# Performance work log

Hardware: AMD Instinct MI355X
Metric: run time of the kernel (lower is better)

Reference implementation:

```python
import jax, jax.numpy as jnp
import numpy as np

DN = ('NCHW', 'OIHW', 'NCHW')
HEADS = 4
EPS_LN = 1e-5
EPS_NORM = 1e-12


def conv(x, w, pad=0, groups=1):
    return jax.lax.conv_general_dilated(
        x, w, window_strides=(1, 1), padding=[(pad, pad), (pad, pad)],
        dimension_numbers=DN, feature_group_count=groups)


def layernorm(x, w, b):
    # LayerNorm over channel axis per spatial position (to_3d -> LN(c) -> to_4d)
    mu = jnp.mean(x, axis=1, keepdims=True)
    var = jnp.mean((x - mu) ** 2, axis=1, keepdims=True)
    return (x - mu) / jnp.sqrt(var + EPS_LN) * w[None, :, None, None] + b[None, :, None, None]


def setup_inputs() -> dict:
    key = jax.random.key(0)
    ks = jax.random.split(key, 12)
    b, dim, h, w = 2, 192, 128, 128
    hidden = int(dim * 2.66)  # 510

    def rn(k, shape, scale=0.05):
        return jax.random.normal(k, shape, dtype=jnp.float32) * scale

    return {
        'x': jax.random.normal(ks[0], (b, dim, h, w), dtype=jnp.float32),
        'illum': jax.random.normal(ks[1], (b, dim, h, w), dtype=jnp.float32),
        'ln1_w': jnp.ones((dim,), jnp.float32), 'ln1_b': jnp.zeros((dim,), jnp.float32),
        'lnL_w': jnp.ones((dim,), jnp.float32), 'lnL_b': jnp.zeros((dim,), jnp.float32),
        'ln2_w': jnp.ones((dim,), jnp.float32), 'ln2_b': jnp.zeros((dim,), jnp.float32),
        'q_w': rn(ks[2], (dim, dim, 1, 1)),
        'qdw_w': rn(ks[3], (dim, dim, 3, 3)),        # full 3x3 conv (no groups in source)
        'kv_w': rn(ks[4], (2 * dim, dim, 1, 1)),
        'kvdw_w': rn(ks[5], (2 * dim, 1, 3, 3)),     # depthwise, groups = 2*dim
        'temp': jnp.ones((HEADS, 1, 1), jnp.float32),
        'proj_w': rn(ks[6], (dim, dim, 1, 1)),
        'pin_w': rn(ks[7], (hidden, dim, 1, 1)),
        'dw_w': rn(ks[8], (hidden, hidden, 3, 3)),   # full 3x3 conv (no groups in source)
        'pout_w': rn(ks[9], (dim, hidden, 1, 1)),
    }


def _block(x, illum, ln1_w, ln1_b, lnL_w, lnL_b, ln2_w, ln2_b,
           q_w, qdw_w, kv_w, kvdw_w, temp, proj_w, pin_w, dw_w, pout_w):
    b, c, h, w = x.shape
    ch = c // HEADS

    # ---- Illum-guided channel attention (MDTA) ----
    xn = layernorm(x, ln1_w, ln1_b)
    iln = layernorm(illum, lnL_w, lnL_b)
    q = conv(conv(iln, q_w), qdw_w, pad=1)
    kv = conv(conv(xn, kv_w), kvdw_w, pad=1, groups=2 * c)
    k, v = jnp.split(kv, 2, axis=1)

    def split_heads(t):
        return t.reshape(b, HEADS, ch, h * w)  # b head c (hw)

    q, k, v = split_heads(q), split_heads(k), split_heads(v)
    q = q / jnp.maximum(jnp.linalg.norm(q, axis=-1, keepdims=True), EPS_NORM)
    k = k / jnp.maximum(jnp.linalg.norm(k, axis=-1, keepdims=True), EPS_NORM)

    attn = jnp.einsum('bhce,bhde->bhcd', q, k) * temp[None]  # [b, head, ch, ch]
    attn = jax.nn.softmax(attn, axis=-1)
    out = jnp.einsum('bhcd,bhde->bhce', attn, v).reshape(b, c, h, w)
    x = x + conv(out, proj_w)

    # ---- FFN: 1x1 -> full 3x3 -> GELU -> 1x1 ----
    xn2 = layernorm(x, ln2_w, ln2_b)
    f = conv(xn2, pin_w)
    f = jax.nn.gelu(conv(f, dw_w, pad=1), approximate=False)
    x = x + conv(f, pout_w)
    return x


def reference(x, illum, ln1_w, ln1_b, lnL_w, lnL_b, ln2_w, ln2_b,
              q_w, qdw_w, kv_w, kvdw_w, temp, proj_w, pin_w, dw_w, pout_w):
    return _block(x, illum, ln1_w, ln1_b, lnL_w, lnL_b, ln2_w, ln2_b,
                  q_w, qdw_w, kv_w, kvdw_w, temp, proj_w, pin_w, dw_w, pout_w)
```

## Files before the change

kernel.cpp:

```cpp
#include <hip/hip_runtime.h>
#include <hip/hip_bf16.h>

typedef __hip_bfloat16 bf16;
typedef __attribute__((ext_vector_type(8))) short bf16x8v;
typedef __attribute__((ext_vector_type(4))) float f32x4;

namespace {
constexpr int B_  = 2;
constexpr int C_  = 192;
constexpr int HW_ = 128 * 128;
constexpr int C2_ = 384;
}

static __device__ __forceinline__ float fb(bf16 v) { return __bfloat162float(v); }
static __device__ __forceinline__ bf16 tob(float v) { return __float2bfloat16(v); }

typedef __attribute__((address_space(1))) const char GChar;
typedef __attribute__((address_space(3))) char LChar;
static __device__ __forceinline__ void gl16(const void* g, void* l) {
    __builtin_amdgcn_global_load_lds((GChar*)g, (LChar*)l, 16, 0, 0);
}
static __device__ __forceinline__ bf16x8v lread(const bf16* base, int row, int slot) {
    const char* p = (const char*)base + (size_t)row * 128 + ((size_t)((slot ^ (row & 7))) << 4);
    return *(const bf16x8v*)p;
}

static __device__ __forceinline__ void rp1(const float* W, bf16* Wr, int blk, int t,
                                           int N, int K, int Npad, int Kpad) {
    int i = blk * 256 + t;
    if (i >= Npad * Kpad) return;
    int n = i / Kpad, k = i % Kpad;
    float v = (n < N && k < K) ? W[n * K + k] : 0.f;
    Wr[i] = tob(v);
}
static __device__ __forceinline__ void rp3(const float* W, bf16* Wr, int blk, int t,
                                           int N, int K, int Npad, int Kpad) {
    int i = blk * 256 + t;
    int NK = Npad * Kpad;
    if (i >= NK) return;
    int n = i / Kpad, k = i % Kpad;
    if (n < N && k < K) {
        const float* src = W + ((size_t)(n * K + k)) * 9;
#pragma unroll
        for (int q = 0; q < 9; q++) Wr[(size_t)q * NK + i] = tob(src[q]);
    } else {
#pragma unroll
        for (int q = 0; q < 9; q++) Wr[(size_t)q * NK + i] = tob(0.f);
    }
}
__global__ __launch_bounds__(256) void k_repack_all(
    const float* __restrict__ qw, const float* __restrict__ kvw,
    const float* __restrict__ projw, const float* __restrict__ pinw,
    const float* __restrict__ poutw, const float* __restrict__ qdww,
    const float* __restrict__ dww,
    bf16* __restrict__ Wq1, bf16* __restrict__ Wkv, bf16* __restrict__ Wproj,
    bf16* __restrict__ Wpin, bf16* __restrict__ Wpout, bf16* __restrict__ Wqdw,
    bf16* __restrict__ Wdw, char* __restrict__ zpage) {
    int blk = blockIdx.x, t = threadIdx.x;
    if (blk < 144)        rp1(qw,    Wq1,   blk,        t, 192, 192, 192, 192);
    else if (blk < 432)   rp1(kvw,   Wkv,   blk - 144,  t, 384, 192, 384, 192);
    else if (blk < 576)   rp1(projw, Wproj, blk - 432,  t, 192, 192, 192, 192);
    else if (blk < 960)   rp1(pinw,  Wpin,  blk - 576,  t, 510, 192, 512, 192);
    else if (blk < 1344)  rp1(poutw, Wpout, blk - 960,  t, 192, 510, 192, 512);
    else if (blk < 1488)  rp3(qdww,  Wqdw,  blk - 1344, t, 192, 192, 192, 192);
    else if (blk < 2512)  rp3(dww,   Wdw,   blk - 1488, t, 510, 510, 512, 512);
    else ((uint4*)zpage)[t] = make_uint4(0u, 0u, 0u, 0u);
}

__global__ __launch_bounds__(256) void k_ln_nchw(const float* __restrict__ X0,
                                                 const float* __restrict__ X1,
                                                 const float* __restrict__ w0,
                                                 const float* __restrict__ b0,
                                                 const float* __restrict__ w1,
                                                 const float* __restrict__ b1,
                                                 bf16* __restrict__ out0,
                                                 bf16* __restrict__ out1) {
    const float* X = blockIdx.y ? X1 : X0;
    const float* w = blockIdx.y ? w1 : w0;
    const float* bb = blockIdx.y ? b1 : b0;
    bf16* out = blockIdx.y ? out1 : out0;
    __shared__ float lds[64][C_ + 1];
    int t = threadIdx.x;
    int p0 = blockIdx.x * 64;
    int b = p0 / HW_, pi0 = p0 % HW_;
    for (int i = t; i < 64 * C_; i += 256) {
        int c = i >> 6, pp = i & 63;
        lds[pp][c] = X[((size_t)(b * C_ + c)) * HW_ + pi0 + pp];
    }
    __syncthreads();
    int pp = t >> 2, qq = t & 3;
    float s = 0.f, s2 = 0.f;
    for (int c = qq * 48; c < qq * 48 + 48; c++) { float v = lds[pp][c]; s += v; s2 += v * v; }
    s  += __shfl_xor(s, 1);  s  += __shfl_xor(s, 2);
    s2 += __shfl_xor(s2, 1); s2 += __shfl_xor(s2, 2);
    float mu = s / C_;
    float rstd = rsqrtf(s2 / C_ - mu * mu + 1e-5f);
    size_t ob = ((size_t)(p0 + pp)) * C_;
    for (int c = qq * 48; c < qq * 48 + 48; c++)
        out[ob + c] = tob((lds[pp][c] - mu) * rstd * w[c] + bb[c]);
}

__global__ __launch_bounds__(256) void k_ln_pc(const bf16* __restrict__ X2,
                                               const float* __restrict__ w,
                                               const float* __restrict__ bb,
                                               bf16* __restrict__ out) {
    int t = threadIdx.x;
    int p = blockIdx.x * 64 + (t >> 2), qq = t & 3;
    const bf16* row = X2 + (size_t)p * C_;
    float s = 0.f, s2 = 0.f;
    for (int c = qq * 48; c < qq * 48 + 48; c++) { float v = fb(row[c]); s += v; s2 += v * v; }
    s  += __shfl_xor(s, 1);  s  += __shfl_xor(s, 2);
    s2 += __shfl_xor(s2, 1); s2 += __shfl_xor(s2, 2);
    float mu = s / C_;
    float rstd = rsqrtf(s2 / C_ - mu * mu + 1e-5f);
    bf16* orow = out + (size_t)p * C_;
    for (int c = qq * 48; c < qq * 48 + 48; c++)
        orow[c] = tob((fb(row[c]) - mu) * rstd * w[c] + bb[c]);
}

template <int BN, int EPI>
__global__ __launch_bounds__(256) void k_gemm1x1(const bf16* __restrict__ A,
                                                 const bf16* __restrict__ Wr,
                                                 const int K, const int Cout,
                                                 void* __restrict__ outp,
                                                 const void* __restrict__ resid,
                                                 const int wbstride) {
    constexpr int WN = BN / 2, FN = WN / 16, BIT = BN / 32;
    __shared__ __align__(16) bf16 As[128 * 64];
    __shared__ __align__(16) bf16 Bs[BN * 64];
    const int t = threadIdx.x;
    const int mt = blockIdx.x;
    const int n0 = blockIdx.y * BN;
    const int b = mt >> 7, y = mt & 127;
    const int w = t >> 6, lane = t & 63;
    const int wm = w >> 1, wn = w & 1;
    const int g = lane >> 4, r = lane & 15;
    const int ldw = t - lane;

    f32x4 acc[4][FN];
#pragma unroll
    for (int i = 0; i < 4; i++)
#pragma unroll
        for (int j = 0; j < FN; j++) acc[i][j] = {0.f, 0.f, 0.f, 0.f};

    const bf16* Abase = A + (size_t)mt * 128 * K;
    const bf16* Wbase = Wr + (size_t)b * wbstride;

    for (int c0 = 0; c0 < K; c0 += 64) {
#pragma unroll
        for (int it = 0; it < 4; it++) {
            int idx = it * 256 + t;
            int row = idx >> 3, sl = idx & 7;
            const char* gp = (const char*)(Abase + (size_t)row * K + c0) + ((sl ^ (row & 7)) << 4);
            gl16(gp, (char*)As + (size_t)(it * 256 + ldw) * 16);
        }
#pragma unroll
        for (int it = 0; it < BIT; it++) {
            int idx = it * 256 + t;
            int row = idx >> 3, sl = idx & 7;
            const char* gp = (const char*)(Wbase + (size_t)(n0 + row) * K + c0) + ((sl ^ (row & 7)) << 4);
            gl16(gp, (char*)Bs + (size_t)(it * 256 + ldw) * 16);
        }
        __syncthreads();
#pragma unroll
        for (int ks = 0; ks < 2; ks++) {
            bf16x8v af[4], bv[FN];
#pragma unroll
            for (int fm = 0; fm < 4; fm++)
                af[fm] = lread(As, wm * 64 + fm * 16 + r, ks * 4 + g);
#pragma unroll
            for (int fn = 0; fn < FN; fn++)
                bv[fn] = lread(Bs, wn * WN + fn * 16 + r, ks * 4 + g);
#pragma unroll
            for (int fm = 0; fm < 4; fm++)
#pragma unroll
                for (int fn = 0; fn < FN; fn++)
                    acc[fm][fn] = __builtin_amdgcn_mfma_f32_16x16x32_bf16(af[fm], bv[fn], acc[fm][fn], 0, 0, 0);
        }
        __syncthreads();
    }

#pragma unroll
    for (int fm = 0; fm < 4; fm++)
#pragma unroll
        for (int fn = 0; fn < FN; fn++)
#pragma unroll
            for (int reg = 0; reg < 4; reg++) {
                int xl = wm * 64 + fm * 16 + g * 4 + reg;
                int co = n0 + wn * WN + fn * 16 + r;
                float v = acc[fm][fn][reg];
                if constexpr (EPI == 1) {
                    ((bf16*)outp)[((size_t)mt * 128 + xl) * Cout + co] = tob(v);
                } else if constexpr (EPI == 2) {
                    v += ((const float*)resid)[((size_t)(b * C_ + co)) * HW_ + y * 128 + xl];
                    ((bf16*)outp)[((size_t)mt * 128 + xl) * C_ + co] = tob(v);
                } else {
                    v += fb(((const bf16*)resid)[((size_t)mt * 128 + xl) * C_ + co]);
                    ((float*)outp)[((size_t)(b * C_ + co)) * HW_ + y * 128 + xl] = v;
                }
            }
}

template <int BN, int EPI>
__global__ __launch_bounds__(256) void k_gemm3x3(const bf16* __restrict__ A,
                                                 const bf16* __restrict__ Wr,
                                                 const int Cin, const int Cout,
                                                 bf16* __restrict__ outp,
                                                 const char* __restrict__ zpage) {
    constexpr int WN = BN / 2, FN = WN / 16, BIT = BN / 32;
    __shared__ __align__(16) bf16 As[160 * 64];
    __shared__ __align__(16) bf16 Bs[BN * 64];
    const int t = threadIdx.x;
    const int mtRaw = blockIdx.x;
    const int mt = ((mtRaw & 7) << 5) | (mtRaw >> 3);
    const int n0 = blockIdx.y * BN;
    const int b = mt >> 7, y = mt & 127;
    const int w = t >> 6, lane = t & 63;
    const int wm = w >> 1, wn = w & 1;
    const int g = lane >> 4, r = lane & 15;
    const int ldw = t - lane;

    f32x4 acc[4][FN];
#pragma unroll
    for (int i = 0; i < 4; i++)
#pragma unroll
        for (int j = 0; j < FN; j++) acc[i][j] = {0.f, 0.f, 0.f, 0.f};

    for (int ky = 0; ky < 3; ky++) {
        const int yy = y + ky - 1;
        if (yy < 0 || yy > 127) continue;
        const bf16* Ab = A + ((size_t)b * HW_ + (size_t)yy * 128) * Cin;
        for (int c0 = 0; c0 < Cin; c0 += 64) {
            for (int kx = 0; kx < 3; kx++) {
                if (kx == 0) {
#pragma unroll
                    for (int it = 0; it < 5; it++) {
                        int idx = it * 256 + t;
                        int row = idx >> 3, sl = idx & 7;
                        int so = (sl ^ (row & 7)) << 4;
                        const char* gp = (row >= 1 && row <= 128)
                            ? (const char*)(Ab + (size_t)(row - 1) * Cin + c0) + so
                            : zpage + so;
                        gl16(gp, (char*)As + (size_t)(it * 256 + ldw) * 16);
                    }
                }
                const bf16* Wb = Wr + (size_t)(ky * 3 + kx) * Cout * Cin;
#pragma unroll
                for (int it = 0; it < BIT; it++) {
                    int idx = it * 256 + t;
                    int row = idx >> 3, sl = idx & 7;
                    const char* gp = (const char*)(Wb + (size_t)(n0 + row) * Cin + c0) + ((sl ^ (row & 7)) << 4);
                    gl16(gp, (char*)Bs + (size_t)(it * 256 + ldw) * 16);
                }
                __syncthreads();
#pragma unroll
                for (int ks = 0; ks < 2; ks++) {
                    bf16x8v af[4], bv[FN];
#pragma unroll
                    for (int fm = 0; fm < 4; fm++)
                        af[fm] = lread(As, wm * 64 + fm * 16 + r + kx, ks * 4 + g);
#pragma unroll
                    for (int fn = 0; fn < FN; fn++)
                        bv[fn] = lread(Bs, wn * WN + fn * 16 + r, ks * 4 + g);
#pragma unroll
                    for (int fm = 0; fm < 4; fm++)
#pragma unroll
                        for (int fn = 0; fn < FN; fn++)
                            acc[fm][fn] = __builtin_amdgcn_mfma_f32_16x16x32_bf16(af[fm], bv[fn], acc[fm][fn], 0, 0, 0);
                }
                __syncthreads();
            }
        }
    }
#pragma unroll
    for (int fm = 0; fm < 4; fm++)
#pragma unroll
        for (int fn = 0; fn < FN; fn++)
#pragma unroll
            for (int reg = 0; reg < 4; reg++) {
                int xl = wm * 64 + fm * 16 + g * 4 + reg;
                int co = n0 + wn * WN + fn * 16 + r;
                float v = acc[fm][fn][reg];
                if constexpr (EPI == 1) v = 0.5f * v * (1.0f + erff(v * 0.70710678118654752f));
                outp[((size_t)mt * 128 + xl) * Cout + co] = tob(v);
            }
}

__global__ __launch_bounds__(192) void k_dwconv2(const bf16* __restrict__ kv,
                                                 const float* __restrict__ wdw,
                                                 bf16* __restrict__ kout,
                                                 bf16* __restrict__ vout) {
    __shared__ float wlds[1728];
    const int t = threadIdx.x;
    const int row = blockIdx.x;
    const int z = blockIdx.y;
    const int b = row >> 7, y = row & 127;
    for (int i = t; i < 432; i += 192)
        ((float4*)wlds)[i] = ((const float4*)(wdw + (size_t)z * 1728))[i];
    __syncthreads();
    const int c8h = t % 24, xg = t / 24;
    const int cbase = z * C_ + c8h * 8;
    float wreg[9][8];
#pragma unroll
    for (int tap = 0; tap < 9; tap++)
#pragma unroll
        for (int j = 0; j < 8; j++) wreg[tap][j] = wlds[(c8h * 8 + j) * 9 + tap];

    bf16* outb = (z == 0 ? kout : vout) + (size_t)(b * HW_ + y * 128) * C_ + c8h * 8;
    const uint4 zero4 = make_uint4(0u, 0u, 0u, 0u);
    for (int i = 0; i < 16; i++) {
        int x = xg + 8 * i;
        float acc[8];
#pragma unroll
        for (int j = 0; j < 8; j++) acc[j] = 0.f;
#pragma unroll
        for (int ky = 0; ky < 3; ky++) {
            int yy = y + ky - 1;
            if (yy < 0 || yy > 127) continue;
            const bf16* rb = kv + ((size_t)b * HW_ + (size_t)yy * 128) * C2_ + cbase;
#pragma unroll
            for (int kx = 0; kx < 3; kx++) {
                int xx = x + kx - 1;
                uint4 vv = (xx >= 0 && xx <= 127) ? *(const uint4*)(rb + (size_t)xx * C2_) : zero4;
                const bf16* pv = (const bf16*)&vv;
#pragma unroll
                for (int j = 0; j < 8; j++)
                    acc[j] += fb(pv[j]) * wreg[ky * 3 + kx][j];
            }
        }
        union { bf16 h[8]; uint4 u; } ov;
#pragma unroll
        for (int j = 0; j < 8; j++) ov.h[j] = tob(acc[j]);
        *(uint4*)(outb + (size_t)x * C_) = ov.u;
    }
}

__global__ __launch_bounds__(192) void k_ssqpart(const bf16* __restrict__ q,
                                                 const bf16* __restrict__ k,
                                                 float* __restrict__ ssq) {
    __shared__ float red[192][8];
    int t = threadIdx.x;
    int c8 = t % 24, slot = t / 24;
    int ch = blockIdx.x, b = blockIdx.y, sel = blockIdx.z;
    const bf16* src = (sel ? k : q) + ((size_t)b * HW_ + ch * 256) * C_ + c8 * 8;
    float s[8];
#pragma unroll
    for (int j = 0; j < 8; j++) s[j] = 0.f;
    for (int i = slot; i < 256; i += 8) {
        uint4 v = *(const uint4*)(src + (size_t)i * C_);
        const bf16* pv = (const bf16*)&v;
#pragma unroll
        for (int j = 0; j < 8; j++) { float x = fb(pv[j]); s[j] += x * x; }
    }
#pragma unroll
    for (int j = 0; j < 8; j++) red[t][j] = s[j];
    __syncthreads();
    if (slot == 0) {
        float o[8];
#pragma unroll
        for (int j = 0; j < 8; j++) o[j] = 0.f;
        for (int ss = 0; ss < 8; ss++)
#pragma unroll
            for (int j = 0; j < 8; j++) o[j] += red[c8 + 24 * ss][j];
        float* dst = ssq + (((size_t)(sel * 2 + b)) * 64 + ch) * C_ + c8 * 8;
#pragma unroll
        for (int j = 0; j < 8; j++) dst[j] = o[j];
    }
}

__global__ __launch_bounds__(256) void k_qk(const bf16* __restrict__ q,
                                            const bf16* __restrict__ k,
                                            float* __restrict__ Spart) {
    __shared__ float qs[64][49];
    __shared__ float ks[64][49];
    int t = threadIdx.x;
    int ch = blockIdx.x, hd = blockIdx.y, b = blockIdx.z;
    int i0 = (t >> 4) * 3, j0 = (t & 15) * 3;
    float acc[3][3];
#pragma unroll
    for (int a = 0; a < 3; a++)
#pragma unroll
        for (int c = 0; c < 3; c++) acc[a][c] = 0.f;

    for (int sub = 0; sub < 4; sub++) {
        size_t rbase = ((size_t)b * HW_ + ch * 256 + sub * 64) * C_ + hd * 48;
        for (int i = t; i < 64 * 6; i += 256) {
            int row = i / 6, oc = i % 6;
            uint4 v = *(const uint4*)(q + rbase + (size_t)row * C_ + oc * 8);
            const bf16* pv = (const bf16*)&v;
#pragma unroll
            for (int j = 0; j < 8; j++) qs[row][oc * 8 + j] = fb(pv[j]);
            uint4 v2 = *(const uint4*)(k + rbase + (size_t)row * C_ + oc * 8);
            const bf16* pv2 = (const bf16*)&v2;
#pragma unroll
            for (int j = 0; j < 8; j++) ks[row][oc * 8 + j] = fb(pv2[j]);
        }
        __syncthreads();
        for (int p = 0; p < 64; p++) {
            float a0 = qs[p][i0], a1 = qs[p][i0 + 1], a2 = qs[p][i0 + 2];
            float b0 = ks[p][j0], b1 = ks[p][j0 + 1], b2 = ks[p][j0 + 2];
            acc[0][0] += a0 * b0; acc[0][1] += a0 * b1; acc[0][2] += a0 * b2;
            acc[1][0] += a1 * b0; acc[1][1] += a1 * b1; acc[1][2] += a1 * b2;
            acc[2][0] += a2 * b0; acc[2][1] += a2 * b1; acc[2][2] += a2 * b2;
        }
        __syncthreads();
    }
    float* dst = Spart + (((size_t)(b * 4 + hd)) * 64 + ch) * 2304;
#pragma unroll
    for (int a = 0; a < 3; a++)
#pragma unroll
        for (int c = 0; c < 3; c++) dst[(i0 + a) * 48 + (j0 + c)] = acc[a][c];
}

__global__ __launch_bounds__(256) void k_softmax(const float* __restrict__ Spart,
                                                 const float* __restrict__ ssq,
                                                 const float* __restrict__ temp,
                                                 bf16* __restrict__ attnW) {
    __shared__ float S[2304];
    __shared__ float invk_s[48];
    int t = threadIdx.x;
    int hd = blockIdx.x, b = blockIdx.y;
    const float* base = Spart + ((size_t)(b * 4 + hd)) * 64 * 2304;
    for (int e = t; e < 2304; e += 256) {
        float s = 0.f;
        for (int ch = 0; ch < 64; ch++) s += base[(size_t)ch * 2304 + e];
        S[e] = s;
    }
    if (t < 48) {
        int c = hd * 48 + t;
        float sk = 0.f;
        for (int ch = 0; ch < 64; ch++) sk += ssq[((size_t)(2 + b) * 64 + ch) * C_ + c];
        invk_s[t] = 1.f / fmaxf(sqrtf(sk), 1e-12f);
    }
    __syncthreads();
    if (t >= 48) return;
    int c = hd * 48 + t;
    float sq = 0.f;
    for (int ch = 0; ch < 64; ch++) sq += ssq[((size_t)b * 64 + ch) * C_ + c];
    float qi = 1.f / fmaxf(sqrtf(sq), 1e-12f);
    float tp = temp[hd];
    float row[48];
    float mx = -1e30f;
    for (int j = 0; j < 48; j++) {
        float s = S[t * 48 + j] * qi * invk_s[j] * tp;
        row[j] = s;
        mx = fmaxf(mx, s);
    }
    float sum = 0.f;
    for (int j = 0; j < 48; j++) { row[j] = expf(row[j] - mx); sum += row[j]; }
    float is = 1.f / sum;
    bf16* wrow = attnW + ((size_t)b * 192 + hd * 48 + t) * 192;
    for (int blk4 = 0; blk4 < 4; blk4++)
        for (int j = 0; j < 48; j++)
            wrow[blk4 * 48 + j] = tob(blk4 == hd ? row[j] * is : 0.f);
}

extern "C" void kernel_launch(void* const* d_in, const int* in_sizes, int n_in,
                              void* d_out, int out_size, void* d_ws, size_t ws_size,
                              hipStream_t stream) {
    const float* x     = (const float*)d_in[0];
    const float* illum = (const float*)d_in[1];
    const float* ln1w  = (const float*)d_in[2];
    const float* ln1b  = (const float*)d_in[3];
    const float* lnLw  = (const float*)d_in[4];
    const float* lnLb  = (const float*)d_in[5];
    const float* ln2w  = (const float*)d_in[6];
    const float* ln2b  = (const float*)d_in[7];
    const float* qw    = (const float*)d_in[8];
    const float* qdww  = (const float*)d_in[9];
    const float* kvw   = (const float*)d_in[10];
    const float* kvdww = (const float*)d_in[11];
    const float* temp  = (const float*)d_in[12];
    const float* projw = (const float*)d_in[13];
    const float* pinw  = (const float*)d_in[14];
    const float* dww   = (const float*)d_in[15];
    const float* poutw = (const float*)d_in[16];

    char* ws = (char*)d_ws;
    bf16*  Wq1   = (bf16*)(ws + 0);
    bf16*  Wkv   = (bf16*)(ws + 73728);
    bf16*  Wqdw  = (bf16*)(ws + 221184);
    bf16*  Wproj = (bf16*)(ws + 884736);
    bf16*  Wpin  = (bf16*)(ws + 958464);
    bf16*  Wdw   = (bf16*)(ws + 1155072);
    bf16*  Wpout = (bf16*)(ws + 5873664);
    float* ssq   = (float*)(ws + 6070272);
    char*  zpage = (char*)(ws + 6266880);
    const size_t A0 = 6270976, u = 12582912;
    bf16* xn    = (bf16*)(ws + A0 + 0 * u);
    bf16* iln   = (bf16*)(ws + A0 + 1 * u);
    bf16* qtmp  = (bf16*)(ws + A0 + 2 * u);
    bf16* qb    = (bf16*)(ws + A0 + 1 * u);
    bf16* kvtmp = (bf16*)(ws + A0 + 2 * u);
    bf16* kb    = (bf16*)(ws + A0 + 0 * u);
    bf16* vb    = (bf16*)(ws + A0 + 4 * u);
    float* Spart = (float*)(ws + A0 + 3 * u);
    bf16*  attnW = (bf16*)(ws + A0 + 3 * u + 4718592);
    bf16* outa  = (bf16*)(ws + A0 + 2 * u);
    bf16* x2    = (bf16*)(ws + A0 + 0 * u);
    bf16* xn2   = (bf16*)(ws + A0 + 3 * u);
    bf16* fbuf  = (bf16*)(ws + A0 + 4 * u);
    bf16* gbuf  = (bf16*)(ws + A0 + 1 * u);

    k_repack_all<<<2513, 256, 0, stream>>>(qw, kvw, projw, pinw, poutw, qdww, dww,
                                           Wq1, Wkv, Wproj, Wpin, Wpout, Wqdw, Wdw, zpage);

    k_ln_nchw<<<dim3(512, 2), 256, 0, stream>>>(x, illum, ln1w, ln1b, lnLw, lnLb, xn, iln);

    k_gemm1x1<96, 1><<<dim3(256, 2), 256, 0, stream>>>(iln, Wq1, 192, 192, qtmp, nullptr, 0);
    k_gemm3x3<96, 0><<<dim3(256, 2), 256, 0, stream>>>(qtmp, Wqdw, 192, 192, qb, zpage);

    k_gemm1x1<128, 1><<<dim3(256, 3), 256, 0, stream>>>(xn, Wkv, 192, 384, kvtmp, nullptr, 0);
    k_dwconv2<<<dim3(256, 2), 192, 0, stream>>>(kvtmp, kvdww, kb, vb);

    k_ssqpart<<<dim3(64, 2, 2), 192, 0, stream>>>(qb, kb, ssq);
    k_qk<<<dim3(64, 4, 2), 256, 0, stream>>>(qb, kb, Spart);
    k_softmax<<<dim3(4, 2), 256, 0, stream>>>(Spart, ssq, temp, attnW);
    k_gemm1x1<96, 1><<<dim3(256, 2), 256, 0, stream>>>(vb, attnW, 192, 192, outa, nullptr, 36864);

    k_gemm1x1<96, 2><<<dim3(256, 2), 256, 0, stream>>>(outa, Wproj, 192, 192, x2, x, 0);

    k_ln_pc<<<512, 256, 0, stream>>>(x2, ln2w, ln2b, xn2);
    k_gemm1x1<128, 1><<<dim3(256, 4), 256, 0, stream>>>(xn2, Wpin, 192, 512, fbuf, nullptr, 0);
    k_gemm3x3<128, 1><<<dim3(256, 4), 256, 0, stream>>>(fbuf, Wdw, 512, 512, gbuf, zpage);
    k_gemm1x1<96, 3><<<dim3(256, 2), 256, 0, stream>>>(gbuf, Wpout, 512, 192, d_out, x2, 0);
}
```

Baseline: 406.6 us.

## Vectorize layernorm I/O, slide dwconv window, fuse sum-of-squares into qk kernel

Layernorm kernels now read the NCHW input as float4, keep the bf16 per-channel rows in registers, and write 16-byte packed bf16 stores instead of scalar accesses. The depthwise conv gives each thread a contiguous run of 16 pixels and keeps a 3x3 register window that slides along x, so each input vector is loaded once instead of three times. The separate q/k sum-of-squares kernel is removed and its reduction is folded into k_qk, which already stages the same tiles in LDS. This saves one launch and a full re-read of q and k, at the cost of a little extra LDS work and another barrier inside k_qk.

```diff
diff --git a/kernel.cpp b/kernel.cpp
--- a/kernel.cpp
+++ b/kernel.cpp
@@ -83,9 +83,11 @@
     int t = threadIdx.x;
     int p0 = blockIdx.x * 64;
     int b = p0 / HW_, pi0 = p0 % HW_;
-    for (int i = t; i < 64 * C_; i += 256) {
-        int c = i >> 6, pp = i & 63;
-        lds[pp][c] = X[((size_t)(b * C_ + c)) * HW_ + pi0 + pp];
+    for (int i = t; i < 64 * C_ / 4; i += 256) {
+        int c = i >> 4, pp4 = (i & 15) << 2;
+        float4 v = *(const float4*)(X + ((size_t)(b * C_ + c)) * HW_ + pi0 + pp4);
+        lds[pp4 + 0][c] = v.x; lds[pp4 + 1][c] = v.y;
+        lds[pp4 + 2][c] = v.z; lds[pp4 + 3][c] = v.w;
     }
     __syncthreads();
     int pp = t >> 2, qq = t & 3;
@@ -95,9 +97,17 @@
     s2 += __shfl_xor(s2, 1); s2 += __shfl_xor(s2, 2);
     float mu = s / C_;
     float rstd = rsqrtf(s2 / C_ - mu * mu + 1e-5f);
-    size_t ob = ((size_t)(p0 + pp)) * C_;
-    for (int c = qq * 48; c < qq * 48 + 48; c++)
-        out[ob + c] = tob((lds[pp][c] - mu) * rstd * w[c] + bb[c]);
+    bf16* ob = out + ((size_t)(p0 + pp)) * C_ + qq * 48;
+#pragma unroll
+    for (int j = 0; j < 6; j++) {
+        union { bf16 h[8]; uint4 u; } ov;
+#pragma unroll
+        for (int e = 0; e < 8; e++) {
+            int c = qq * 48 + j * 8 + e;
+            ov.h[e] = tob((lds[pp][c] - mu) * rstd * w[c] + bb[c]);
+        }
+        *(uint4*)(ob + j * 8) = ov.u;
+    }
 }
 
 __global__ __launch_bounds__(256) void k_ln_pc(const bf16* __restrict__ X2,
@@ -106,16 +116,33 @@
                                                bf16* __restrict__ out) {
     int t = threadIdx.x;
     int p = blockIdx.x * 64 + (t >> 2), qq = t & 3;
-    const bf16* row = X2 + (size_t)p * C_;
+    const bf16* row = X2 + (size_t)p * C_ + qq * 48;
+    uint4 u[6];
+#pragma unroll
+    for (int j = 0; j < 6; j++) u[j] = *(const uint4*)(row + j * 8);
     float s = 0.f, s2 = 0.f;
-    for (int c = qq * 48; c < qq * 48 + 48; c++) { float v = fb(row[c]); s += v; s2 += v * v; }
+#pragma unroll
+    for (int j = 0; j < 6; j++) {
+        const bf16* pv = (const bf16*)&u[j];
+#pragma unroll
+        for (int e = 0; e < 8; e++) { float v = fb(pv[e]); s += v; s2 += v * v; }
+    }
     s  += __shfl_xor(s, 1);  s  += __shfl_xor(s, 2);
     s2 += __shfl_xor(s2, 1); s2 += __shfl_xor(s2, 2);
     float mu = s / C_;
     float rstd = rsqrtf(s2 / C_ - mu * mu + 1e-5f);
-    bf16* orow = out + (size_t)p * C_;
-    for (int c = qq * 48; c < qq * 48 + 48; c++)
-        orow[c] = tob((fb(row[c]) - mu) * rstd * w[c] + bb[c]);
+    bf16* orow = out + (size_t)p * C_ + qq * 48;
+#pragma unroll
+    for (int j = 0; j < 6; j++) {
+        const bf16* pv = (const bf16*)&u[j];
+        union { bf16 h[8]; uint4 u4; } ov;
+#pragma unroll
+        for (int e = 0; e < 8; e++) {
+            int c = qq * 48 + j * 8 + e;
+            ov.h[e] = tob((fb(pv[e]) - mu) * rstd * w[c] + bb[c]);
+        }
+        *(uint4*)(orow + j * 8) = ov.u4;
+    }
 }
 
 template <int BN, int EPI>
@@ -308,75 +335,60 @@
 
     bf16* outb = (z == 0 ? kout : vout) + (size_t)(b * HW_ + y * 128) * C_ + c8h * 8;
     const uint4 zero4 = make_uint4(0u, 0u, 0u, 0u);
+    const int x0 = xg * 16;
+    bool vy[3]; const bf16* rowp[3];
+#pragma unroll
+    for (int ky = 0; ky < 3; ky++) {
+        int yy = y + ky - 1;
+        vy[ky] = (yy >= 0 && yy <= 127);
+        int yyc = vy[ky] ? yy : 0;
+        rowp[ky] = kv + ((size_t)b * HW_ + (size_t)yyc * 128) * C2_ + cbase;
+    }
+    uint4 win[3][3];
+#pragma unroll
+    for (int ky = 0; ky < 3; ky++) {
+        win[ky][0] = (vy[ky] && x0 - 1 >= 0) ? *(const uint4*)(rowp[ky] + (size_t)(x0 - 1) * C2_) : zero4;
+        win[ky][1] = vy[ky] ? *(const uint4*)(rowp[ky] + (size_t)x0 * C2_) : zero4;
+    }
     for (int i = 0; i < 16; i++) {
-        int x = xg + 8 * i;
+        int x = x0 + i;
+#pragma unroll
+        for (int ky = 0; ky < 3; ky++)
+            win[ky][2] = (vy[ky] && x + 1 <= 127) ? *(const uint4*)(rowp[ky] + (size_t)(x + 1) * C2_) : zero4;
         float acc[8];
 #pragma unroll
         for (int j = 0; j < 8; j++) acc[j] = 0.f;
 #pragma unroll
-        for (int ky = 0; ky < 3; ky++) {
-            int yy = y + ky - 1;
-            if (yy < 0 || yy > 127) continue;
-            const bf16* rb = kv + ((size_t)b * HW_ + (size_t)yy * 128) * C2_ + cbase;
+        for (int ky = 0; ky < 3; ky++)
 #pragma unroll
             for (int kx = 0; kx < 3; kx++) {
-                int xx = x + kx - 1;
-                uint4 vv = (xx >= 0 && xx <= 127) ? *(const uint4*)(rb + (size_t)xx * C2_) : zero4;
-                const bf16* pv = (const bf16*)&vv;
+                const bf16* pv = (const bf16*)&win[ky][kx];
 #pragma unroll
                 for (int j = 0; j < 8; j++)
                     acc[j] += fb(pv[j]) * wreg[ky * 3 + kx][j];
             }
-        }
         union { bf16 h[8]; uint4 u; } ov;
 #pragma unroll
         for (int j = 0; j < 8; j++) ov.h[j] = tob(acc[j]);
         *(uint4*)(outb + (size_t)x * C_) = ov.u;
-    }
-}
-
-__global__ __launch_bounds__(192) void k_ssqpart(const bf16* __restrict__ q,
-                                                 const bf16* __restrict__ k,
-                                                 float* __restrict__ ssq) {
-    __shared__ float red[192][8];
-    int t = threadIdx.x;
-    int c8 = t % 24, slot = t / 24;
-    int ch = blockIdx.x, b = blockIdx.y, sel = blockIdx.z;
-    const bf16* src = (sel ? k : q) + ((size_t)b * HW_ + ch * 256) * C_ + c8 * 8;
-    float s[8];
-#pragma unroll
-    for (int j = 0; j < 8; j++) s[j] = 0.f;
-    for (int i = slot; i < 256; i += 8) {
-        uint4 v = *(const uint4*)(src + (size_t)i * C_);
-        const bf16* pv = (const bf16*)&v;
-#pragma unroll
-        for (int j = 0; j < 8; j++) { float x = fb(pv[j]); s[j] += x * x; }
-    }
-#pragma unroll
-    for (int j = 0; j < 8; j++) red[t][j] = s[j];
-    __syncthreads();
-    if (slot == 0) {
-        float o[8];
-#pragma unroll
-        for (int j = 0; j < 8; j++) o[j] = 0.f;
-        for (int ss = 0; ss < 8; ss++)
-#pragma unroll
-            for (int j = 0; j < 8; j++) o[j] += red[c8 + 24 * ss][j];
-        float* dst = ssq + (((size_t)(sel * 2 + b)) * 64 + ch) * C_ + c8 * 8;
-#pragma unroll
-        for (int j = 0; j < 8; j++) dst[j] = o[j];
+#pragma unroll
+        for (int ky = 0; ky < 3; ky++) { win[ky][0] = win[ky][1]; win[ky][1] = win[ky][2]; }
     }
 }
 
 __global__ __launch_bounds__(256) void k_qk(const bf16* __restrict__ q,
                                             const bf16* __restrict__ k,
-                                            float* __restrict__ Spart) {
+                                            float* __restrict__ Spart,
+                                            float* __restrict__ ssq) {
     __shared__ float qs[64][49];
     __shared__ float ks[64][49];
+    __shared__ float redq[4][48], redk[4][48];
     int t = threadIdx.x;
     int ch = blockIdx.x, hd = blockIdx.y, b = blockIdx.z;
     int i0 = (t >> 4) * 3, j0 = (t & 15) * 3;
+    int cs = t % 48, qr = t / 48;
     float acc[3][3];
+    float sq = 0.f, sk = 0.f;
 #pragma unroll
     for (int a = 0; a < 3; a++)
 #pragma unroll
@@ -396,6 +408,13 @@
             for (int j = 0; j < 8; j++) ks[row][oc * 8 + j] = fb(pv2[j]);
         }
         __syncthreads();
+        if (t < 192) {
+#pragma unroll
+            for (int rr = 0; rr < 16; rr++) {
+                float qv = qs[qr * 16 + rr][cs]; sq += qv * qv;
+                float kv2 = ks[qr * 16 + rr][cs]; sk += kv2 * kv2;
+            }
+        }
         for (int p = 0; p < 64; p++) {
             float a0 = qs[p][i0], a1 = qs[p][i0 + 1], a2 = qs[p][i0 + 2];
             float b0 = ks[p][j0], b1 = ks[p][j0 + 1], b2 = ks[p][j0 + 2];
@@ -405,11 +424,19 @@
         }
         __syncthreads();
     }
+    if (t < 192) { redq[qr][cs] = sq; redk[qr][cs] = sk; }
     float* dst = Spart + (((size_t)(b * 4 + hd)) * 64 + ch) * 2304;
 #pragma unroll
     for (int a = 0; a < 3; a++)
 #pragma unroll
         for (int c = 0; c < 3; c++) dst[(i0 + a) * 48 + (j0 + c)] = acc[a][c];
+    __syncthreads();
+    if (t < 48) {
+        float s0 = redq[0][t] + redq[1][t] + redq[2][t] + redq[3][t];
+        float s1 = redk[0][t] + redk[1][t] + redk[2][t] + redk[3][t];
+        ssq[((size_t)b * 64 + ch) * C_ + hd * 48 + t] = s0;
+        ssq[((size_t)(2 + b) * 64 + ch) * C_ + hd * 48 + t] = s1;
+    }
 }
 
 __global__ __launch_bounds__(256) void k_softmax(const float* __restrict__ Spart,
@@ -513,8 +540,7 @@
     k_gemm1x1<128, 1><<<dim3(256, 3), 256, 0, stream>>>(xn, Wkv, 192, 384, kvtmp, nullptr, 0);
     k_dwconv2<<<dim3(256, 2), 192, 0, stream>>>(kvtmp, kvdww, kb, vb);
 
-    k_ssqpart<<<dim3(64, 2, 2), 192, 0, stream>>>(qb, kb, ssq);
-    k_qk<<<dim3(64, 4, 2), 256, 0, stream>>>(qb, kb, Spart);
+    k_qk<<<dim3(64, 4, 2), 256, 0, stream>>>(qb, kb, Spart, ssq);
     k_softmax<<<dim3(4, 2), 256, 0, stream>>>(Spart, ssq, temp, attnW);
     k_gemm1x1<96, 1><<<dim3(256, 2), 256, 0, stream>>>(vb, attnW, 192, 192, outa, nullptr, 36864);
 
```

New measurement: 380.8 us. -6.4%, faster.
